# Kernel optimization log

Measured on AMD Instinct MI355X. Metric: run time of the kernel, lower is better.

## Reference

```python
import jax, jax.numpy as jnp
import numpy as np

COMPONENTS = 16
INPUT_DIM = 128
STAGE_NUM = 10
BETA = 3.0
EPS = 1e-6


def setup_inputs() -> dict:
    key = jax.random.key(0)
    k1, k2 = jax.random.split(key)
    embeddings = jax.random.normal(k1, (65536, INPUT_DIM), dtype=jnp.float32)
    means = jax.random.normal(k2, (COMPONENTS, INPUT_DIM), dtype=jnp.float32)
    covariances = jnp.tile(jnp.eye(INPUT_DIM, dtype=jnp.float32)[None], (COMPONENTS, 1, 1))
    return {"embeddings": embeddings, "means": means, "covariances": covariances}


def _em(embeddings, means, covs):
    """Run STAGE_NUM EM stages; return (last memberships z [N,K], final means [K,D])."""
    N, D = embeddings.shape
    K = means.shape[0]
    log_prior = jnp.log(jnp.full((K,), 1.0 / K, dtype=embeddings.dtype) + EPS)  # uniform, non-trainable
    eye = jnp.eye(D, dtype=embeddings.dtype)
    log_2pi = jnp.log(jnp.asarray(2.0 * np.pi, dtype=embeddings.dtype))

    def step(carry, _):
        means, covs = carry
        # E-step: batched Cholesky + triangular solve for Mahalanobis distance
        chol = jnp.linalg.cholesky(covs + EPS * eye)                         # [K,D,D]
        diff = embeddings[None, :, :] - means[:, None, :]                    # [K,N,D]
        sol = jax.scipy.linalg.solve_triangular(
            chol, diff.transpose(0, 2, 1), lower=True)                       # [K,D,N]
        maha = jnp.sum(sol * sol, axis=1)                                    # [K,N]
        logdet = 2.0 * jnp.sum(jnp.log(jnp.diagonal(chol, axis1=-2, axis2=-1)), axis=-1)  # [K]
        logp = -0.5 * (D * log_2pi + logdet[:, None] + maha) + log_prior[:, None]          # [K,N]
        z = jax.nn.softmax(logp, axis=0).T                                   # [N,K]
        # M-step (each component's update independent, matching torch loop)
        tw = jnp.sum(z, axis=0)                                              # [K]
        new_means = (z.T @ embeddings) / (tw[:, None] + EPS)                 # [K,D]
        d2 = embeddings[None, :, :] - new_means[:, None, :]                  # [K,N,D]
        new_covs = jnp.einsum('kn,knd,kne->kde', z.T, d2, d2) / (tw[:, None, None] + EPS)
        return (new_means, new_covs), z

    (means_f, _covs_f), zs = jax.lax.scan(step, (means, covs), None, length=STAGE_NUM)
    return zs[-1], means_f


def reference(embeddings, means, covariances):
    z, means_f = _em(embeddings, means, covariances)
    out = BETA * (z @ means_f) + embeddings
    return out, z
```

## Files before the change

kernel.cpp:

```cpp
#include <hip/hip_runtime.h>
#include <math.h>


#define NPTS 65536
#define DIM 128
#define KC 16
#define STAGES 10
#define BETA_C 3.0f
#define EPS_C 1e-6f
#define NCHG 16
#define GCH (NPTS / NCHG)

typedef __attribute__((ext_vector_type(8))) short bfrag_t;
typedef __attribute__((ext_vector_type(16))) float f32x16;

__device__ __forceinline__ unsigned short bf_hi(float f) {
  unsigned u = __float_as_uint(f);
  return (unsigned short)((u + 0x7fffu + ((u >> 16) & 1u)) >> 16);
}
__device__ __forceinline__ float bf_f(unsigned short h) {
  return __uint_as_float((unsigned)h << 16);
}
__device__ __forceinline__ bfrag_t bc(int4 v) {
  return __builtin_bit_cast(bfrag_t, v);
}

#define SPLIT_PACK(V0, V1, V2, V3, V4, V5, V6, V7, HI, LO)                    \
  {                                                                           \
    const unsigned short h0 = bf_hi(V0), h1 = bf_hi(V1), h2 = bf_hi(V2),      \
                         h3 = bf_hi(V3), h4 = bf_hi(V4), h5 = bf_hi(V5),      \
                         h6 = bf_hi(V6), h7 = bf_hi(V7);                      \
    (HI).x = (int)((unsigned)h0 | ((unsigned)h1 << 16));                      \
    (HI).y = (int)((unsigned)h2 | ((unsigned)h3 << 16));                      \
    (HI).z = (int)((unsigned)h4 | ((unsigned)h5 << 16));                      \
    (HI).w = (int)((unsigned)h6 | ((unsigned)h7 << 16));                      \
    const unsigned short l0 = bf_hi((V0) - bf_f(h0)),                         \
                         l1 = bf_hi((V1) - bf_f(h1)),                         \
                         l2 = bf_hi((V2) - bf_f(h2)),                         \
                         l3 = bf_hi((V3) - bf_f(h3)),                         \
                         l4 = bf_hi((V4) - bf_f(h4)),                         \
                         l5 = bf_hi((V5) - bf_f(h5)),                         \
                         l6 = bf_hi((V6) - bf_f(h6)),                         \
                         l7 = bf_hi((V7) - bf_f(h7));                         \
    (LO).x = (int)((unsigned)l0 | ((unsigned)l1 << 16));                      \
    (LO).y = (int)((unsigned)l2 | ((unsigned)l3 << 16));                      \
    (LO).z = (int)((unsigned)l4 | ((unsigned)l5 << 16));                      \
    (LO).w = (int)((unsigned)l6 | ((unsigned)l7 << 16));                      \
  }

__global__ __launch_bounds__(256) void xsplit_kernel(
    const float* __restrict__ X, int4* __restrict__ XBh, int4* __restrict__ XBl)
{
  const int nb = blockIdx.x;
  const int t = threadIdx.x;
  const int e = t >> 1, h = t & 1;
  float v[8];
#pragma unroll
  for (int j = 0; j < 8; ++j)
    v[j] = X[(size_t)(nb * 16 + h * 8 + j) * DIM + e];
  int4 hi, lo;
  SPLIT_PACK(v[0], v[1], v[2], v[3], v[4], v[5], v[6], v[7], hi, lo)
  const size_t idx = ((size_t)nb * DIM + e) * 2 + h;
  XBh[idx] = hi;
  XBl[idx] = lo;
}

__global__ __launch_bounds__(256) void prep_kernel(
    const float* __restrict__ covs, const float* __restrict__ means,
    int4* __restrict__ WBh, int4* __restrict__ WBl,
    float* __restrict__ mvec, float* __restrict__ kconst)
{
  extern __shared__ float smem[];
  float (*A)[DIM + 1]  = (float (*)[DIM + 1])smem;
  float (*Wv)[DIM + 1] = (float (*)[DIM + 1])(smem + 16512);
  float (*T)[65]       = (float (*)[65])(smem + 33024);
  float* red = smem + 37184;

  const int k = blockIdx.x;
  const int t = threadIdx.x;
  const int lane = t & 63;
  const int wv = t >> 6;
  const float* C = covs + (size_t)k * DIM * DIM;

  {
    const int tr = t & 127, th = t >> 7;
    for (int i = th; i < DIM; i += 2) {
      float v = C[(size_t)i * DIM + tr];
      if (i == tr) v += EPS_C;
      A[i][tr] = v;
      Wv[i][tr] = 0.0f;
    }
  }
  __syncthreads();

  for (int b = 0; b < 8; ++b) {
    const int o = b * 16;
    if (wv == 0) {
      const int l = lane;
      for (int j = 0; j < 16; ++j) {
        const float djj = sqrtf(A[o + j][o + j]);
        if (l == j) A[o + j][o + j] = djj;
        if (l > j && l < 16) {
          A[o + l][o + j] /= djj;
          const float f = A[o + l][o + j];
          for (int c = j + 1; c <= l; ++c)
            A[o + l][o + c] -= f * A[o + c][o + j];
        }
      }
    }
    __syncthreads();
    const int nr = DIM - o - 16;
    if (nr > 0) {
      if (t < nr) {
        const int i = o + 16 + t;
        float li[16];
#pragma unroll
        for (int c = 0; c < 16; ++c) {
          float s = A[i][o + c];
#pragma unroll
          for (int p = 0; p < c; ++p) s -= li[p] * A[o + c][o + p];
          li[c] = s / A[o + c][o + c];
          A[i][o + c] = li[c];
        }
      }
      __syncthreads();
      {
        const int ir = t >> 1, half = t & 1;
        if (ir < nr) {
          const int i = o + 16 + ir;
          float li[16];
#pragma unroll
          for (int p = 0; p < 16; ++p) li[p] = A[i][o + p];
          for (int j = o + 16 + half; j <= i; j += 2) {
            float s = A[i][j];
#pragma unroll
            for (int p = 0; p < 16; ++p) s -= li[p] * A[j][o + p];
            A[i][j] = s;
          }
        }
      }
      __syncthreads();
    }
  }

  if (t < DIM) {
    const int g = t >> 6, c = t & 63, o = g * 64;
    Wv[o + c][o + c] = 1.0f / A[o + c][o + c];
    for (int i = c + 1; i < 64; ++i) {
      float s = 0.0f;
      for (int p = c; p < i; ++p) s += A[o + i][o + p] * Wv[o + p][o + c];
      Wv[o + i][o + c] = -s / A[o + i][o + i];
    }
  }
  __syncthreads();
  for (int idx = t; idx < 4096; idx += 256) {
    const int i = idx >> 6, c = idx & 63;
    float s = 0.0f;
    for (int p = c; p < 64; ++p) s += A[64 + i][p] * Wv[p][c];
    T[i][c] = s;
  }
  __syncthreads();
  for (int idx = t; idx < 4096; idx += 256) {
    const int i = idx >> 6, c = idx & 63;
    float s = 0.0f;
    for (int p = 0; p <= i; ++p) s += Wv[64 + i][64 + p] * T[p][c];
    Wv[64 + i][c] = -s;
  }
  __syncthreads();

  if (t < DIM) {
    const float* mu = means + k * DIM;
    float s = 0.0f;
    for (int e = 0; e <= t; ++e) s += Wv[t][e] * mu[e];
    mvec[k * DIM + t] = s;
    red[t] = logf(A[t][t]);
  }
  __syncthreads();
  if (t == 0) {
    float s = 0.0f;
    for (int i = 0; i < DIM; ++i) s += red[i];
    kconst[k] = -s;
  }
  {
    const int d = t & 127, h = t >> 7;
#pragma unroll
    for (int es = 0; es < 8; ++es) {
      float v[8];
#pragma unroll
      for (int j = 0; j < 8; ++j) v[j] = Wv[d][es * 16 + h * 8 + j];
      int4 hi, lo;
      SPLIT_PACK(v[0], v[1], v[2], v[3], v[4], v[5], v[6], v[7], hi, lo)
      const size_t idx = ((size_t)(k * 8 + es) * DIM + d) * 2 + h;
      WBh[idx] = hi;
      WBl[idx] = lo;
    }
  }
}

#define EST_DT(DT)                                                            \
  {                                                                           \
    f32x16 accv;                                                              \
    _Pragma("unroll") for (int r = 0; r < 16; ++r) accv[r] = 0.0f;            \
    _Pragma("unroll") for (int es = 0; es < 2 * (DT) + 2; ++es) {             \
      const size_t wb = ((size_t)(k * 8 + es) * DIM + (DT) * 32 + c31) * 2 + hh; \
      const int4 bh = WBh[wb];                                                \
      const int4 bl = WBl[wb];                                                \
      accv = __builtin_amdgcn_mfma_f32_32x32x16_bf16(bc(axl[es]), bc(bh), accv, 0, 0, 0); \
      accv = __builtin_amdgcn_mfma_f32_32x32x16_bf16(bc(axh[es]), bc(bl), accv, 0, 0, 0); \
      accv = __builtin_amdgcn_mfma_f32_32x32x16_bf16(bc(axh[es]), bc(bh), accv, 0, 0, 0); \
    }                                                                         \
    const float mval = mvec[k * DIM + (DT) * 32 + c31];                       \
    _Pragma("unroll") for (int r = 0; r < 16; ++r) {                          \
      const float v = accv[r] - mval;                                         \
      part[r] = fmaf(v, v, part[r]);                                          \
    }                                                                         \
  }

__global__ __launch_bounds__(256, 2) void estep_kernel(
    const float* __restrict__ X, const int4* __restrict__ WBh,
    const int4* __restrict__ WBl, const float* __restrict__ mvec,
    const float* __restrict__ kconst, float* __restrict__ Z,
    float* __restrict__ Zt)
{
  __shared__ int4 XAh[8][128][2];
  __shared__ int4 XAl[8][128][2];
  float (*lp)[KC + 1] = (float (*)[KC + 1]) & XAh[0][0][0];

  const int tid = threadIdx.x;
  const int c31 = tid & 31;
  const int hh = (tid & 63) >> 5;
  const int w = tid >> 6;
  const size_t n0 = (size_t)blockIdx.x * 128;

  {
    const int n = tid & 127, h2 = tid >> 7;
    const int hsw = h2 ^ ((n >> 2) & 1);
    const float4* xr = (const float4*)(X + (n0 + n) * DIM);
#pragma unroll
    for (int es = 0; es < 8; ++es) {
      const float4 a = xr[es * 4 + h2 * 2];
      const float4 b = xr[es * 4 + h2 * 2 + 1];
      int4 hi, lo;
      SPLIT_PACK(a.x, a.y, a.z, a.w, b.x, b.y, b.z, b.w, hi, lo)
      XAh[es][n][hsw] = hi;
      XAl[es][n][hsw] = lo;
    }
  }
  __syncthreads();

  int4 axh[8], axl[8];
  {
    const int nl = w * 32 + c31;
    const int hsw = hh ^ ((nl >> 2) & 1);
#pragma unroll
    for (int es = 0; es < 8; ++es) {
      axh[es] = XAh[es][nl][hsw];
      axl[es] = XAl[es][nl][hsw];
    }
  }
  __syncthreads();

  for (int k = 0; k < KC; ++k) {
    float part[16];
#pragma unroll
    for (int r = 0; r < 16; ++r) part[r] = 0.0f;
    EST_DT(0)
    EST_DT(1)
    EST_DT(2)
    EST_DT(3)
#pragma unroll
    for (int off = 1; off < 32; off <<= 1) {
#pragma unroll
      for (int r = 0; r < 16; ++r) part[r] += __shfl_xor(part[r], off, 64);
    }
    float sel = 0.0f;
#pragma unroll
    for (int r = 0; r < 16; ++r) sel = (c31 == r) ? part[r] : sel;
    if (c31 < 16) {
      const int row = (c31 & 3) + 8 * (c31 >> 2) + 4 * hh;
      lp[w * 32 + row][k] = kconst[k] - 0.5f * sel;
    }
  }
  __syncthreads();

  if (tid < 128) {
    float v[KC];
    float mx = -1e30f;
#pragma unroll
    for (int q = 0; q < KC; ++q) { v[q] = lp[tid][q]; mx = fmaxf(mx, v[q]); }
    float s = 0.0f;
#pragma unroll
    for (int q = 0; q < KC; ++q) { v[q] = expf(v[q] - mx); s += v[q]; }
    const float inv = 1.0f / s;
    float4* zr = (float4*)(Z + (n0 + tid) * KC);
#pragma unroll
    for (int q = 0; q < KC / 4; ++q)
      zr[q] = make_float4(v[4 * q] * inv, v[4 * q + 1] * inv,
                          v[4 * q + 2] * inv, v[4 * q + 3] * inv);
#pragma unroll
    for (int q = 0; q < KC; ++q)
      Zt[(size_t)q * NPTS + n0 + tid] = v[q] * inv;
  }
}

__global__ __launch_bounds__(256, 4) void gram_kernel(
    const float* __restrict__ Zt, const int4* __restrict__ XBh,
    const int4* __restrict__ XBl, float* __restrict__ Gp,
    float* __restrict__ sp, float* __restrict__ twp)
{
  const int k = blockIdx.x;
  const int ch = blockIdx.y;
  const int dh = blockIdx.z;
  const int tid = threadIdx.x;
  const int c31 = tid & 31;
  const int hh = (tid & 63) >> 5;
  const int w = tid >> 6;
  const int dt = w & 1;
  const int et0 = (w >> 1) * 2;
  const int drd = dh * 64 + dt * 32 + c31;
  const int n0 = ch * GCH;
  const float* __restrict__ zrow = Zt + (size_t)k * NPTS;

  f32x16 acc0, acc1;
#pragma unroll
  for (int r = 0; r < 16; ++r) { acc0[r] = 0.0f; acc1[r] = 0.0f; }
  float sacc = 0.0f, twacc = 0.0f;

#pragma unroll 2
  for (int nb = 0; nb < GCH / 16; ++nb) {
    const size_t nb16 = (size_t)(ch * (GCH / 16)) + nb;
    const size_t ai = (nb16 * DIM + drd) * 2 + hh;
    const int4 xh = XBh[ai];
    const int4 xl = XBl[ai];
    const float4 z0 = *(const float4*)(zrow + n0 + nb * 16 + hh * 8);
    const float4 z1 = *(const float4*)(zrow + n0 + nb * 16 + hh * 8 + 4);
    float p[8];
    {
      const unsigned wx0 = (unsigned)xh.x, wl0 = (unsigned)xl.x;
      const unsigned wx1 = (unsigned)xh.y, wl1 = (unsigned)xl.y;
      const unsigned wx2 = (unsigned)xh.z, wl2 = (unsigned)xl.z;
      const unsigned wx3 = (unsigned)xh.w, wl3 = (unsigned)xl.w;
      p[0] = z0.x * (__uint_as_float(wx0 << 16) + __uint_as_float(wl0 << 16));
      p[1] = z0.y * (__uint_as_float(wx0 & 0xffff0000u) + __uint_as_float(wl0 & 0xffff0000u));
      p[2] = z0.z * (__uint_as_float(wx1 << 16) + __uint_as_float(wl1 << 16));
      p[3] = z0.w * (__uint_as_float(wx1 & 0xffff0000u) + __uint_as_float(wl1 & 0xffff0000u));
      p[4] = z1.x * (__uint_as_float(wx2 << 16) + __uint_as_float(wl2 << 16));
      p[5] = z1.y * (__uint_as_float(wx2 & 0xffff0000u) + __uint_as_float(wl2 & 0xffff0000u));
      p[6] = z1.z * (__uint_as_float(wx3 << 16) + __uint_as_float(wl3 << 16));
      p[7] = z1.w * (__uint_as_float(wx3 & 0xffff0000u) + __uint_as_float(wl3 & 0xffff0000u));
    }
    sacc += ((p[0] + p[1]) + (p[2] + p[3])) + ((p[4] + p[5]) + (p[6] + p[7]));
    twacc += ((z0.x + z0.y) + (z0.z + z0.w)) + ((z1.x + z1.y) + (z1.z + z1.w));
    int4 ah, al;
    SPLIT_PACK(p[0], p[1], p[2], p[3], p[4], p[5], p[6], p[7], ah, al)
    const size_t b0 = (nb16 * DIM + (et0 + 0) * 32 + c31) * 2 + hh;
    const size_t b1 = (nb16 * DIM + (et0 + 1) * 32 + c31) * 2 + hh;
    {
      const int4 bh = XBh[b0], bl = XBl[b0];
      acc0 = __builtin_amdgcn_mfma_f32_32x32x16_bf16(bc(al), bc(bh), acc0, 0, 0, 0);
      acc0 = __builtin_amdgcn_mfma_f32_32x32x16_bf16(bc(ah), bc(bl), acc0, 0, 0, 0);
      acc0 = __builtin_amdgcn_mfma_f32_32x32x16_bf16(bc(ah), bc(bh), acc0, 0, 0, 0);
    }
    {
      const int4 bh = XBh[b1], bl = XBl[b1];
      acc1 = __builtin_amdgcn_mfma_f32_32x32x16_bf16(bc(al), bc(bh), acc1, 0, 0, 0);
      acc1 = __builtin_amdgcn_mfma_f32_32x32x16_bf16(bc(ah), bc(bl), acc1, 0, 0, 0);
      acc1 = __builtin_amdgcn_mfma_f32_32x32x16_bf16(bc(ah), bc(bh), acc1, 0, 0, 0);
    }
  }

  {
    float* gbase = Gp + (size_t)(ch * KC + k) * (DIM * DIM);
#pragma unroll
    for (int r = 0; r < 16; ++r) {
      const int row = (r & 3) + 8 * (r >> 2) + 4 * hh;
      const int d = dh * 64 + dt * 32 + row;
      gbase[(size_t)d * DIM + (et0 + 0) * 32 + c31] = acc0[r];
      gbase[(size_t)d * DIM + (et0 + 1) * 32 + c31] = acc1[r];
    }
  }

  sacc += __shfl_xor(sacc, 32, 64);
  if (w < 2 && hh == 0)
    sp[(size_t)(ch * KC + k) * DIM + dt * 32 + c31 + dh * 64] = sacc;
  twacc += __shfl_xor(twacc, 32, 64);
  if (dh == 0 && tid == 0) twp[ch * KC + k] = twacc;
}

__global__ __launch_bounds__(256) void reduce_means_kernel(
    const float* __restrict__ sp, const float* __restrict__ twp,
    float* __restrict__ means, float* __restrict__ tw_out)
{
  const int idx = blockIdx.x * 256 + threadIdx.x;
  const int k = idx >> 7;
  float tw = 0.0f;
#pragma unroll
  for (int c = 0; c < NCHG; ++c) tw += twp[c * KC + k];
  float s = 0.0f;
  for (int c = 0; c < NCHG; ++c) s += sp[(size_t)c * KC * DIM + idx];
  means[idx] = s / (tw + EPS_C);
  if ((idx & 127) == 0) tw_out[k] = tw;
}

__global__ __launch_bounds__(256) void finalize_cov_kernel(
    const float* __restrict__ Gp, const float* __restrict__ means,
    const float* __restrict__ tw_in, float* __restrict__ covs)
{
  const int idx = blockIdx.x * 256 + threadIdx.x;
  const int k = idx >> 14;
  const int d = (idx >> 7) & 127;
  const int e = idx & 127;
  float g = 0.0f;
  for (int c = 0; c < NCHG; ++c)
    g += Gp[(size_t)(c * KC + k) * (DIM * DIM) + d * DIM + e];
  const float tw = tw_in[k];
  const float denom = tw + EPS_C;
  const float md = means[k * DIM + d], me = means[k * DIM + e];
  covs[idx] = g / denom - ((tw + 2.0f * EPS_C) / denom) * md * me;
}

__global__ __launch_bounds__(256) void out_kernel(
    const float* __restrict__ X, const float* __restrict__ Z,
    const float* __restrict__ means, float* __restrict__ out)
{
  const int i4 = blockIdx.x * 256 + threadIdx.x;
  const int n = i4 >> 5;
  const int q = i4 & 31;
  float4 acc = ((const float4*)X)[i4];
  const float* zr = Z + (size_t)n * KC;
#pragma unroll
  for (int k = 0; k < KC; ++k) {
    const float zk = BETA_C * zr[k];
    const float4 mu = ((const float4*)means)[k * 32 + q];
    acc.x = fmaf(zk, mu.x, acc.x);
    acc.y = fmaf(zk, mu.y, acc.y);
    acc.z = fmaf(zk, mu.z, acc.z);
    acc.w = fmaf(zk, mu.w, acc.w);
  }
  ((float4*)out)[i4] = acc;
}

extern "C" void kernel_launch(void* const* d_in, const int* in_sizes, int n_in,
                              void* d_out, int out_size, void* d_ws, size_t ws_size,
                              hipStream_t stream)
{
  const float* X = (const float*)d_in[0];
  const float* means0 = (const float*)d_in[1];
  const float* covs0 = (const float*)d_in[2];
  float* out = (float*)d_out;
  float* Zout = out + (size_t)NPTS * DIM;

  int4* XBh = (int4*)out;
  int4* XBl = XBh + (size_t)(NPTS / 16) * DIM * 2;

  char* p = (char*)d_ws;
  float* covs_cur  = (float*)p;  p += (size_t)262144 * 4;
  float* mvec      = (float*)p;  p += 2048 * 4;
  float* kconst    = (float*)p;  p += 64;
  float* tw        = (float*)p;  p += 64;
  float* means_cur = (float*)p;  p += 2048 * 4;
  float* sp        = (float*)p;  p += (size_t)NCHG * KC * DIM * 4;
  float* twp       = (float*)p;  p += NCHG * KC * 4;
  int4* WBh        = (int4*)p;   p += (size_t)KC * 8 * DIM * 2 * 16;
  int4* WBl        = (int4*)p;   p += (size_t)KC * 8 * DIM * 2 * 16;
  float* Zt        = (float*)p;  p += (size_t)KC * NPTS * 4;
  float* Gp        = (float*)p;  p += (size_t)NCHG * KC * DIM * DIM * 4;

  const int prep_lds = 37312 * 4;
  (void)hipFuncSetAttribute((const void*)prep_kernel,
      hipFuncAttributeMaxDynamicSharedMemorySize, prep_lds);

  xsplit_kernel<<<NPTS / 16, 256, 0, stream>>>(X, XBh, XBl);

  for (int s = 0; s < STAGES; ++s) {
    const float* cs = (s == 0) ? covs0 : covs_cur;
    const float* ms = (s == 0) ? means0 : means_cur;
    prep_kernel<<<KC, 256, prep_lds, stream>>>(cs, ms, WBh, WBl, mvec, kconst);
    estep_kernel<<<NPTS / 128, 256, 0, stream>>>(X, WBh, WBl, mvec, kconst,
                                                 Zout, Zt);
    gram_kernel<<<dim3(KC, NCHG, 2), 256, 0, stream>>>(Zt, XBh, XBl, Gp, sp, twp);
    reduce_means_kernel<<<8, 256, 0, stream>>>(sp, twp, means_cur, tw);
    if (s < STAGES - 1)
      finalize_cov_kernel<<<KC * DIM * DIM / 256, 256, 0, stream>>>(
          Gp, means_cur, tw, covs_cur);
  }
  out_kernel<<<(NPTS * DIM / 4) / 256, 256, 0, stream>>>(X, Zout, means_cur, out);
}
```

Before: 5.885 ms.

## Restructure gram kernel: full-width tiles, atomic accumulation, skip last-stage covariance

The gram kernel drops the two-way split over the d dimension, so each block computes all 128x128 outputs with four accumulators per wave and computes the A-operand products once instead of twice. Partial Gram matrices are now accumulated with float atomics into one buffer, which is zeroed by a memset, instead of being written per chunk and summed in finalize. The chunk count doubles to keep enough blocks in flight. The last stage skips the unused covariance entirely by running a lightweight moment kernel. The bf16 hi/lo split now uses the packed convert instruction. The costs are atomic contention, a lower occupancy bound, and run-to-run nondeterminism in the summation order.

```diff
diff --git a/kernel.cpp b/kernel.cpp
--- a/kernel.cpp
+++ b/kernel.cpp
@@ -8,7 +8,7 @@
 #define STAGES 10
 #define BETA_C 3.0f
 #define EPS_C 1e-6f
-#define NCHG 16
+#define NCHG 32
 #define GCH (NPTS / NCHG)
 
 typedef __attribute__((ext_vector_type(8))) short bfrag_t;
@@ -48,6 +48,18 @@
     (LO).w = (int)((unsigned)l6 | ((unsigned)l7 << 16));                      \
   }
 
+__device__ __forceinline__ int cvt_pk2(float a, float b) {
+  int r;
+  asm("v_cvt_pk_bf16_f32 %0, %1, %2" : "=v"(r) : "v"(a), "v"(b));
+  return r;
+}
+__device__ __forceinline__ void cvt_split2(float a, float b, int& hi, int& lo) {
+  hi = cvt_pk2(a, b);
+  const float fa = __uint_as_float((unsigned)hi << 16);
+  const float fb = __uint_as_float((unsigned)hi & 0xffff0000u);
+  lo = cvt_pk2(a - fa, b - fb);
+}
+
 __global__ __launch_bounds__(256) void xsplit_kernel(
     const float* __restrict__ X, int4* __restrict__ XBh, int4* __restrict__ XBl)
 {
@@ -303,88 +315,115 @@
   }
 }
 
-__global__ __launch_bounds__(256, 4) void gram_kernel(
+#define GR_ET(ACC, ET)                                                        \
+  {                                                                           \
+    const size_t bi = (nbg * DIM + (ET) * 32 + c31) * 2 + hh;                 \
+    const int4 bh = XBh[bi], bl = XBl[bi];                                    \
+    ACC = __builtin_amdgcn_mfma_f32_32x32x16_bf16(bc(al), bc(bh), ACC, 0, 0, 0); \
+    ACC = __builtin_amdgcn_mfma_f32_32x32x16_bf16(bc(ah), bc(bl), ACC, 0, 0, 0); \
+    ACC = __builtin_amdgcn_mfma_f32_32x32x16_bf16(bc(ah), bc(bh), ACC, 0, 0, 0); \
+  }
+
+__global__ __launch_bounds__(256, 2) void gram_kernel(
     const float* __restrict__ Zt, const int4* __restrict__ XBh,
     const int4* __restrict__ XBl, float* __restrict__ Gp,
     float* __restrict__ sp, float* __restrict__ twp)
 {
   const int k = blockIdx.x;
   const int ch = blockIdx.y;
-  const int dh = blockIdx.z;
   const int tid = threadIdx.x;
   const int c31 = tid & 31;
   const int hh = (tid & 63) >> 5;
   const int w = tid >> 6;
-  const int dt = w & 1;
-  const int et0 = (w >> 1) * 2;
-  const int drd = dh * 64 + dt * 32 + c31;
+  const int drd = w * 32 + c31;
+  const float* __restrict__ zrow = Zt + (size_t)k * NPTS + ch * GCH;
+
+  f32x16 acc0, acc1, acc2, acc3;
+#pragma unroll
+  for (int r = 0; r < 16; ++r) { acc0[r] = 0.f; acc1[r] = 0.f; acc2[r] = 0.f; acc3[r] = 0.f; }
+  float sacc = 0.0f, twacc = 0.0f;
+
+#pragma unroll 2
+  for (int nb = 0; nb < GCH / 16; ++nb) {
+    const size_t nbg = (size_t)(ch * (GCH / 16)) + nb;
+    const size_t ai = (nbg * DIM + drd) * 2 + hh;
+    const int4 xh = XBh[ai];
+    const int4 xl = XBl[ai];
+    const float4 z0 = *(const float4*)(zrow + nb * 16 + hh * 8);
+    const float4 z1 = *(const float4*)(zrow + nb * 16 + hh * 8 + 4);
+    float p0, p1, p2, p3, p4, p5, p6, p7;
+    {
+      const unsigned a0 = (unsigned)xh.x, b0 = (unsigned)xl.x;
+      const unsigned a1 = (unsigned)xh.y, b1 = (unsigned)xl.y;
+      const unsigned a2 = (unsigned)xh.z, b2 = (unsigned)xl.z;
+      const unsigned a3 = (unsigned)xh.w, b3 = (unsigned)xl.w;
+      p0 = z0.x * (__uint_as_float(a0 << 16) + __uint_as_float(b0 << 16));
+      p1 = z0.y * (__uint_as_float(a0 & 0xffff0000u) + __uint_as_float(b0 & 0xffff0000u));
+      p2 = z0.z * (__uint_as_float(a1 << 16) + __uint_as_float(b1 << 16));
+      p3 = z0.w * (__uint_as_float(a1 & 0xffff0000u) + __uint_as_float(b1 & 0xffff0000u));
+      p4 = z1.x * (__uint_as_float(a2 << 16) + __uint_as_float(b2 << 16));
+      p5 = z1.y * (__uint_as_float(a2 & 0xffff0000u) + __uint_as_float(b2 & 0xffff0000u));
+      p6 = z1.z * (__uint_as_float(a3 << 16) + __uint_as_float(b3 << 16));
+      p7 = z1.w * (__uint_as_float(a3 & 0xffff0000u) + __uint_as_float(b3 & 0xffff0000u));
+    }
+    sacc += ((p0 + p1) + (p2 + p3)) + ((p4 + p5) + (p6 + p7));
+    twacc += ((z0.x + z0.y) + (z0.z + z0.w)) + ((z1.x + z1.y) + (z1.z + z1.w));
+    int4 ah, al;
+    cvt_split2(p0, p1, ah.x, al.x);
+    cvt_split2(p2, p3, ah.y, al.y);
+    cvt_split2(p4, p5, ah.z, al.z);
+    cvt_split2(p6, p7, ah.w, al.w);
+    GR_ET(acc0, 0)
+    GR_ET(acc1, 1)
+    GR_ET(acc2, 2)
+    GR_ET(acc3, 3)
+  }
+
+  {
+    float* gk = Gp + (size_t)k * (DIM * DIM);
+#pragma unroll
+    for (int r = 0; r < 16; ++r) {
+      const int row = (r & 3) + 8 * (r >> 2) + 4 * hh;
+      const int d = w * 32 + row;
+      atomicAdd(&gk[(size_t)d * DIM + 0 * 32 + c31], acc0[r]);
+      atomicAdd(&gk[(size_t)d * DIM + 1 * 32 + c31], acc1[r]);
+      atomicAdd(&gk[(size_t)d * DIM + 2 * 32 + c31], acc2[r]);
+      atomicAdd(&gk[(size_t)d * DIM + 3 * 32 + c31], acc3[r]);
+    }
+  }
+
+  sacc += __shfl_xor(sacc, 32, 64);
+  if (hh == 0) sp[(size_t)(ch * KC + k) * DIM + drd] = sacc;
+  if (w == 0) {
+    twacc += __shfl_xor(twacc, 32, 64);
+    if (tid == 0) twp[ch * KC + k] = twacc;
+  }
+}
+
+__global__ __launch_bounds__(128) void moment_kernel(
+    const float* __restrict__ X, const float* __restrict__ Zt,
+    float* __restrict__ sp, float* __restrict__ twp)
+{
+  __shared__ float red[128];
+  const int k = blockIdx.x;
+  const int ch = blockIdx.y;
+  const int d = threadIdx.x;
   const int n0 = ch * GCH;
   const float* __restrict__ zrow = Zt + (size_t)k * NPTS;
-
-  f32x16 acc0, acc1;
-#pragma unroll
-  for (int r = 0; r < 16; ++r) { acc0[r] = 0.0f; acc1[r] = 0.0f; }
-  float sacc = 0.0f, twacc = 0.0f;
-
-#pragma unroll 2
-  for (int nb = 0; nb < GCH / 16; ++nb) {
-    const size_t nb16 = (size_t)(ch * (GCH / 16)) + nb;
-    const size_t ai = (nb16 * DIM + drd) * 2 + hh;
-    const int4 xh = XBh[ai];
-    const int4 xl = XBl[ai];
-    const float4 z0 = *(const float4*)(zrow + n0 + nb * 16 + hh * 8);
-    const float4 z1 = *(const float4*)(zrow + n0 + nb * 16 + hh * 8 + 4);
-    float p[8];
-    {
-      const unsigned wx0 = (unsigned)xh.x, wl0 = (unsigned)xl.x;
-      const unsigned wx1 = (unsigned)xh.y, wl1 = (unsigned)xl.y;
-      const unsigned wx2 = (unsigned)xh.z, wl2 = (unsigned)xl.z;
-      const unsigned wx3 = (unsigned)xh.w, wl3 = (unsigned)xl.w;
-      p[0] = z0.x * (__uint_as_float(wx0 << 16) + __uint_as_float(wl0 << 16));
-      p[1] = z0.y * (__uint_as_float(wx0 & 0xffff0000u) + __uint_as_float(wl0 & 0xffff0000u));
-      p[2] = z0.z * (__uint_as_float(wx1 << 16) + __uint_as_float(wl1 << 16));
-      p[3] = z0.w * (__uint_as_float(wx1 & 0xffff0000u) + __uint_as_float(wl1 & 0xffff0000u));
-      p[4] = z1.x * (__uint_as_float(wx2 << 16) + __uint_as_float(wl2 << 16));
-      p[5] = z1.y * (__uint_as_float(wx2 & 0xffff0000u) + __uint_as_float(wl2 & 0xffff0000u));
-      p[6] = z1.z * (__uint_as_float(wx3 << 16) + __uint_as_float(wl3 << 16));
-      p[7] = z1.w * (__uint_as_float(wx3 & 0xffff0000u) + __uint_as_float(wl3 & 0xffff0000u));
-    }
-    sacc += ((p[0] + p[1]) + (p[2] + p[3])) + ((p[4] + p[5]) + (p[6] + p[7]));
-    twacc += ((z0.x + z0.y) + (z0.z + z0.w)) + ((z1.x + z1.y) + (z1.z + z1.w));
-    int4 ah, al;
-    SPLIT_PACK(p[0], p[1], p[2], p[3], p[4], p[5], p[6], p[7], ah, al)
-    const size_t b0 = (nb16 * DIM + (et0 + 0) * 32 + c31) * 2 + hh;
-    const size_t b1 = (nb16 * DIM + (et0 + 1) * 32 + c31) * 2 + hh;
-    {
-      const int4 bh = XBh[b0], bl = XBl[b0];
-      acc0 = __builtin_amdgcn_mfma_f32_32x32x16_bf16(bc(al), bc(bh), acc0, 0, 0, 0);
-      acc0 = __builtin_amdgcn_mfma_f32_32x32x16_bf16(bc(ah), bc(bl), acc0, 0, 0, 0);
-      acc0 = __builtin_amdgcn_mfma_f32_32x32x16_bf16(bc(ah), bc(bh), acc0, 0, 0, 0);
-    }
-    {
-      const int4 bh = XBh[b1], bl = XBl[b1];
-      acc1 = __builtin_amdgcn_mfma_f32_32x32x16_bf16(bc(al), bc(bh), acc1, 0, 0, 0);
-      acc1 = __builtin_amdgcn_mfma_f32_32x32x16_bf16(bc(ah), bc(bl), acc1, 0, 0, 0);
-      acc1 = __builtin_amdgcn_mfma_f32_32x32x16_bf16(bc(ah), bc(bh), acc1, 0, 0, 0);
-    }
-  }
-
-  {
-    float* gbase = Gp + (size_t)(ch * KC + k) * (DIM * DIM);
-#pragma unroll
-    for (int r = 0; r < 16; ++r) {
-      const int row = (r & 3) + 8 * (r >> 2) + 4 * hh;
-      const int d = dh * 64 + dt * 32 + row;
-      gbase[(size_t)d * DIM + (et0 + 0) * 32 + c31] = acc0[r];
-      gbase[(size_t)d * DIM + (et0 + 1) * 32 + c31] = acc1[r];
-    }
-  }
-
-  sacc += __shfl_xor(sacc, 32, 64);
-  if (w < 2 && hh == 0)
-    sp[(size_t)(ch * KC + k) * DIM + dt * 32 + c31 + dh * 64] = sacc;
-  twacc += __shfl_xor(twacc, 32, 64);
-  if (dh == 0 && tid == 0) twp[ch * KC + k] = twacc;
+  float s = 0.0f;
+#pragma unroll 4
+  for (int n = n0; n < n0 + GCH; ++n)
+    s = fmaf(zrow[n], X[(size_t)n * DIM + d], s);
+  sp[(size_t)(ch * KC + k) * DIM + d] = s;
+  float tz = 0.0f;
+  for (int i = 0; i < GCH / 128; ++i) tz += zrow[n0 + d + 128 * i];
+  red[d] = tz;
+  __syncthreads();
+  if (d == 0) {
+    float t = 0.0f;
+    for (int i = 0; i < 128; ++i) t += red[i];
+    twp[ch * KC + k] = t;
+  }
 }
 
 __global__ __launch_bounds__(256) void reduce_means_kernel(
@@ -410,9 +449,7 @@
   const int k = idx >> 14;
   const int d = (idx >> 7) & 127;
   const int e = idx & 127;
-  float g = 0.0f;
-  for (int c = 0; c < NCHG; ++c)
-    g += Gp[(size_t)(c * KC + k) * (DIM * DIM) + d * DIM + e];
+  const float g = Gp[idx];
   const float tw = tw_in[k];
   const float denom = tw + EPS_C;
   const float md = means[k * DIM + d], me = means[k * DIM + e];
@@ -464,7 +501,7 @@
   int4* WBh        = (int4*)p;   p += (size_t)KC * 8 * DIM * 2 * 16;
   int4* WBl        = (int4*)p;   p += (size_t)KC * 8 * DIM * 2 * 16;
   float* Zt        = (float*)p;  p += (size_t)KC * NPTS * 4;
-  float* Gp        = (float*)p;  p += (size_t)NCHG * KC * DIM * DIM * 4;
+  float* Gp        = (float*)p;  p += (size_t)KC * DIM * DIM * 4;
 
   const int prep_lds = 37312 * 4;
   (void)hipFuncSetAttribute((const void*)prep_kernel,
@@ -478,7 +515,12 @@
     prep_kernel<<<KC, 256, prep_lds, stream>>>(cs, ms, WBh, WBl, mvec, kconst);
     estep_kernel<<<NPTS / 128, 256, 0, stream>>>(X, WBh, WBl, mvec, kconst,
                                                  Zout, Zt);
-    gram_kernel<<<dim3(KC, NCHG, 2), 256, 0, stream>>>(Zt, XBh, XBl, Gp, sp, twp);
+    if (s < STAGES - 1) {
+      hipMemsetAsync(Gp, 0, (size_t)KC * DIM * DIM * 4, stream);
+      gram_kernel<<<dim3(KC, NCHG), 256, 0, stream>>>(Zt, XBh, XBl, Gp, sp, twp);
+    } else {
+      moment_kernel<<<dim3(KC, NCHG), 128, 0, stream>>>(X, Zt, sp, twp);
+    }
     reduce_means_kernel<<<8, 256, 0, stream>>>(sp, twp, means_cur, tw);
     if (s < STAGES - 1)
       finalize_cov_kernel<<<KC * DIM * DIM / 256, 256, 0, stream>>>(
```

Result: faster. 5.316 ms (-9.7%).
